# Kernel optimization log

Measured on AMD Instinct MI355X. Metric: run time of the kernel, lower is better.

## Reference

```python
import jax, jax.numpy as jnp
import numpy as np

B, L, K = 2, 4096, 32
DIM, PE_DIM, HEADS, DIM_HEAD = 256, 64, 8, 32
INNER = HEADS * DIM_HEAD
SIGMA_INIT = 3.0


def setup_inputs() -> dict:
    key = jax.random.key(0)
    ks = jax.random.split(key, 10)
    x = jax.random.normal(ks[0], (B, L, DIM), dtype=jnp.float32)
    topk_indices = jax.random.randint(ks[1], (B, L, K), 0, L)
    rpe = jax.random.normal(ks[2], (B, L, K, PE_DIM), dtype=jnp.float32)
    distances = jax.random.uniform(ks[3], (B, L, K), dtype=jnp.float32)
    s = lambda fan_in: 1.0 / np.sqrt(fan_in)
    Wq = jax.random.uniform(ks[4], (DIM, INNER), jnp.float32, -s(DIM), s(DIM))
    Wk = jax.random.uniform(ks[5], (DIM + PE_DIM, INNER), jnp.float32, -s(DIM + PE_DIM), s(DIM + PE_DIM))
    Wv = jax.random.uniform(ks[6], (DIM + PE_DIM, INNER), jnp.float32, -s(DIM + PE_DIM), s(DIM + PE_DIM))
    Wout = jax.random.uniform(ks[7], (INNER, DIM), jnp.float32, -s(INNER), s(INNER))
    b_out = jax.random.uniform(ks[8], (DIM,), jnp.float32, -s(INNER), s(INNER))
    log_sigma = jnp.full((HEADS,), np.log(SIGMA_INIT), dtype=jnp.float32)
    return {"x": x, "topk_indices": topk_indices, "rpe": rpe, "distances": distances,
            "Wq": Wq, "Wk": Wk, "Wv": Wv, "Wout": Wout, "b_out": b_out, "log_sigma": log_sigma}


def reference(x, topk_indices, rpe, distances, Wq, Wk, Wv, Wout, b_out, log_sigma):
    H, Dh = HEADS, DIM_HEAD
    scale = Dh ** -0.5
    # per-batch neighbor gather: [B, L, k, D]
    neighbors = jax.vmap(lambda xb, ib: xb[ib])(x, topk_indices)
    context = jnp.concatenate([neighbors, rpe], axis=-1)  # [B, L, k, D+pe]
    Bv, Lv = x.shape[0], x.shape[1]
    Q = (x @ Wq).reshape(Bv, Lv, H, Dh)                       # [B, L, H, d]
    Kt = (context @ Wk).reshape(Bv, Lv, -1, H, Dh)            # [B, L, k, H, d]
    Vt = (context @ Wv).reshape(Bv, Lv, -1, H, Dh)            # [B, L, k, H, d]
    attn = jnp.einsum('blhd,blkhd->bhlk', Q, Kt) * scale      # [B, H, L, k]
    sigma_sq = jnp.exp(log_sigma) ** 2                        # [H]
    bias = -(distances ** 2)[:, None] / (2.0 * sigma_sq[None, :, None, None])
    attn = jax.nn.softmax(attn + bias, axis=-1)
    out = jnp.einsum('bhlk,blkhd->blhd', attn, Vt).reshape(Bv, Lv, H * Dh)
    return out @ Wout + b_out
```

## Files before the change

### kernel.cpp

```cpp
#include <hip/hip_runtime.h>
#include <cstddef>

#define NROWS 8192
#define LLEN  4096
#define KNBR  32
#define DIMX  256
#define PEDIM 64
#define NH    8
#define DHD   32
#define QKVLD 768

__global__ __launch_bounds__(256)
void qkv_gemm(const float* __restrict__ x, const float* __restrict__ Wq,
              const float* __restrict__ Wk, const float* __restrict__ Wv,
              float* __restrict__ QKV)
{
    __shared__ float As[16][64];
    __shared__ float Bs[16][64];
    const int t  = threadIdx.x;
    const int m0 = blockIdx.x * 64;
    const int n0 = blockIdx.y * 64;
    const float* Bmat = (n0 < 256) ? Wq : (n0 < 512) ? Wk : Wv;
    const int nb = n0 & 255;
    const int tx = t & 15, ty = t >> 4;
    const int lm = t >> 2, lk4 = (t & 3) * 4;
    const int bn = t & 63, bk = t >> 6;

    float acc[4][4];
#pragma unroll
    for (int i = 0; i < 4; ++i)
#pragma unroll
        for (int j = 0; j < 4; ++j) acc[i][j] = 0.f;

    for (int k0 = 0; k0 < DIMX; k0 += 16) {
        float4 av = *(const float4*)&x[(size_t)(m0 + lm) * DIMX + k0 + lk4];
        As[lk4 + 0][lm] = av.x;
        As[lk4 + 1][lm] = av.y;
        As[lk4 + 2][lm] = av.z;
        As[lk4 + 3][lm] = av.w;
#pragma unroll
        for (int p = 0; p < 4; ++p)
            Bs[bk + p * 4][bn] = Bmat[(size_t)(k0 + bk + p * 4) * 256 + nb + bn];
        __syncthreads();
#pragma unroll
        for (int kk = 0; kk < 16; ++kk) {
            float4 a = *(const float4*)&As[kk][ty * 4];
            float4 b = *(const float4*)&Bs[kk][tx * 4];
            float ar[4] = {a.x, a.y, a.z, a.w};
            float br[4] = {b.x, b.y, b.z, b.w};
#pragma unroll
            for (int i = 0; i < 4; ++i)
#pragma unroll
                for (int j = 0; j < 4; ++j)
                    acc[i][j] += ar[i] * br[j];
        }
        __syncthreads();
    }
#pragma unroll
    for (int i = 0; i < 4; ++i)
        *(float4*)&QKV[(size_t)(m0 + ty * 4 + i) * QKVLD + n0 + tx * 4] =
            make_float4(acc[i][0], acc[i][1], acc[i][2], acc[i][3]);
}

__global__ __launch_bounds__(256)
void gemm_nn(const float* __restrict__ A, int lda,
             const float* __restrict__ B, int ldb,
             const float* __restrict__ bias,
             float* __restrict__ C, int ldc, int Kd)
{
    __shared__ float As[16][64];
    __shared__ float Bs[16][64];
    const int t  = threadIdx.x;
    const int m0 = blockIdx.x * 64;
    const int n0 = blockIdx.y * 64;
    const int tx = t & 15, ty = t >> 4;
    const int lm = t >> 2, lk4 = (t & 3) * 4;
    const int bn = t & 63, bk = t >> 6;

    float acc[4][4];
#pragma unroll
    for (int i = 0; i < 4; ++i)
#pragma unroll
        for (int j = 0; j < 4; ++j) acc[i][j] = 0.f;

    for (int k0 = 0; k0 < Kd; k0 += 16) {
        float4 av = *(const float4*)&A[(size_t)(m0 + lm) * lda + k0 + lk4];
        As[lk4 + 0][lm] = av.x;
        As[lk4 + 1][lm] = av.y;
        As[lk4 + 2][lm] = av.z;
        As[lk4 + 3][lm] = av.w;
#pragma unroll
        for (int p = 0; p < 4; ++p)
            Bs[bk + p * 4][bn] = B[(size_t)(k0 + bk + p * 4) * ldb + n0 + bn];
        __syncthreads();
#pragma unroll
        for (int kk = 0; kk < 16; ++kk) {
            float4 a = *(const float4*)&As[kk][ty * 4];
            float4 b = *(const float4*)&Bs[kk][tx * 4];
            float ar[4] = {a.x, a.y, a.z, a.w};
            float br[4] = {b.x, b.y, b.z, b.w};
#pragma unroll
            for (int i = 0; i < 4; ++i)
#pragma unroll
                for (int j = 0; j < 4; ++j)
                    acc[i][j] += ar[i] * br[j];
        }
        __syncthreads();
    }
#pragma unroll
    for (int i = 0; i < 4; ++i) {
        const int row = m0 + ty * 4 + i;
        float ov[4];
#pragma unroll
        for (int j = 0; j < 4; ++j)
            ov[j] = acc[i][j] + (bias ? bias[n0 + tx * 4 + j] : 0.f);
        *(float4*)&C[(size_t)row * ldc + n0 + tx * 4] =
            make_float4(ov[0], ov[1], ov[2], ov[3]);
    }
}

__global__ __launch_bounds__(256)
void attn_fused(const float* __restrict__ QKV, const int* __restrict__ topk,
                const float* __restrict__ rpe, const float* __restrict__ dist,
                const float* __restrict__ lsig,
                const float* __restrict__ Wk, const float* __restrict__ Wv,
                float* __restrict__ O)
{
    __shared__ float Qs[4][256];
    __shared__ float Tr[4][NH][PEDIM];
    __shared__ float As2[4][KNBR][NH];
    __shared__ float Us[4][NH][PEDIM];
    __shared__ float Ox[4][256];

    const int t    = threadIdx.x;
    const int w    = t >> 6;
    const int lane = t & 63;
    const int r0   = blockIdx.x * 4;
    const int r    = r0 + w;
    const int b    = r >> 12;
    const float scale = 0.17677669529663687f;

    *(float4*)&Qs[w][lane * 4] = *(const float4*)&QKV[(size_t)r * QKVLD + lane * 4];
    __syncthreads();

    {
        const int h = t >> 5, cl = t & 31;
#pragma unroll
        for (int cc = 0; cc < 2; ++cc) {
            const int c = cl + cc * 32;
            const float4* wp = (const float4*)&Wk[(size_t)(256 + c) * 256 + h * 32];
            float4 wk[8];
#pragma unroll
            for (int j = 0; j < 8; ++j) wk[j] = wp[j];
#pragma unroll
            for (int i = 0; i < 4; ++i) {
                const float4* qp = (const float4*)&Qs[i][h * 32];
                float s = 0.f;
#pragma unroll
                for (int j = 0; j < 8; ++j) {
                    float4 q = qp[j];
                    s += q.x * wk[j].x + q.y * wk[j].y + q.z * wk[j].z + q.w * wk[j].w;
                }
                Tr[i][h][c] = s;
            }
        }
    }
    __syncthreads();

    const int kk = lane & 31, hh = lane >> 5;
    const int myidx = topk[r * KNBR + kk];
    const float* ktrow = &QKV[(size_t)(b * LLEN + myidx) * QKVLD + 256];
    const float* rrow  = &rpe[((size_t)r * KNBR + kk) * PEDIM];

    float acc4[4] = {0.f, 0.f, 0.f, 0.f};
#pragma unroll
    for (int i = 0; i < 4; ++i) {
        const int h = hh * 4 + i;
        const float4* qp = (const float4*)&Qs[w][h * 32];
        const float4* kp = (const float4*)&ktrow[h * 32];
        float s = 0.f;
#pragma unroll
        for (int j = 0; j < 8; ++j) {
            float4 q = qp[j]; float4 kv = kp[j];
            s += q.x * kv.x + q.y * kv.y + q.z * kv.z + q.w * kv.w;
        }
        acc4[i] = s;
    }
    for (int c4 = 0; c4 < 16; ++c4) {
        float4 rv = ((const float4*)rrow)[c4];
#pragma unroll
        for (int i = 0; i < 4; ++i) {
            float4 tv = *(const float4*)&Tr[w][hh * 4 + i][c4 * 4];
            acc4[i] += rv.x * tv.x + rv.y * tv.y + rv.z * tv.z + rv.w * tv.w;
        }
    }
    {
        float dd = dist[r * KNBR + kk];
        const float d2 = dd * dd;
#pragma unroll
        for (int i = 0; i < 4; ++i) {
            const int h = hh * 4 + i;
            const float sig2 = __expf(2.f * lsig[h]);
            float lg = acc4[i] * scale - d2 / (2.f * sig2);
            float mx = lg;
#pragma unroll
            for (int m = 16; m >= 1; m >>= 1)
                mx = fmaxf(mx, __shfl_xor(mx, m, 64));
            float pv = __expf(lg - mx);
            float sm = pv;
#pragma unroll
            for (int m = 16; m >= 1; m >>= 1)
                sm += __shfl_xor(sm, m, 64);
            As2[w][kk][h] = pv / sm;
        }
    }

    {
        const int h2 = lane >> 3;
        const int* tkp = &topk[r * KNBR];
        float4 ox = make_float4(0.f, 0.f, 0.f, 0.f);
        for (int k = 0; k < KNBR; ++k) {
            const int ik = tkp[k];
            const float aw = As2[w][k][h2];
            float4 vv = *(const float4*)&QKV[(size_t)(b * LLEN + ik) * QKVLD + 512 + lane * 4];
            ox.x += aw * vv.x; ox.y += aw * vv.y;
            ox.z += aw * vv.z; ox.w += aw * vv.w;
        }
        *(float4*)&Ox[w][lane * 4] = ox;
    }

    {
        float u[NH] = {0.f, 0.f, 0.f, 0.f, 0.f, 0.f, 0.f, 0.f};
        for (int k = 0; k < KNBR; ++k) {
            const float rv = rpe[((size_t)r * KNBR + k) * PEDIM + lane];
            float4 a0 = *(const float4*)&As2[w][k][0];
            float4 a1 = *(const float4*)&As2[w][k][4];
            u[0] += a0.x * rv; u[1] += a0.y * rv; u[2] += a0.z * rv; u[3] += a0.w * rv;
            u[4] += a1.x * rv; u[5] += a1.y * rv; u[6] += a1.z * rv; u[7] += a1.w * rv;
        }
#pragma unroll
        for (int h = 0; h < NH; ++h) Us[w][h][lane] = u[h];
    }
    __syncthreads();

    {
        const int n = t, hn = n >> 5;
        float accp[4] = {0.f, 0.f, 0.f, 0.f};
        for (int c4 = 0; c4 < 16; ++c4) {
            const float wv0 = Wv[(size_t)(256 + c4 * 4 + 0) * 256 + n];
            const float wv1 = Wv[(size_t)(256 + c4 * 4 + 1) * 256 + n];
            const float wv2 = Wv[(size_t)(256 + c4 * 4 + 2) * 256 + n];
            const float wv3 = Wv[(size_t)(256 + c4 * 4 + 3) * 256 + n];
#pragma unroll
            for (int i = 0; i < 4; ++i) {
                float4 uv = *(const float4*)&Us[i][hn][c4 * 4];
                accp[i] += uv.x * wv0 + uv.y * wv1 + uv.z * wv2 + uv.w * wv3;
            }
        }
#pragma unroll
        for (int i = 0; i < 4; ++i)
            O[(size_t)(r0 + i) * QKVLD + n] = Ox[i][n] + accp[i];
    }
}

extern "C" void kernel_launch(void* const* d_in, const int* in_sizes, int n_in,
                              void* d_out, int out_size, void* d_ws, size_t ws_size,
                              hipStream_t stream)
{
    const float* x     = (const float*)d_in[0];
    const int*   topk  = (const int*)  d_in[1];
    const float* rpe   = (const float*)d_in[2];
    const float* dist  = (const float*)d_in[3];
    const float* Wq    = (const float*)d_in[4];
    const float* Wk    = (const float*)d_in[5];
    const float* Wv    = (const float*)d_in[6];
    const float* Wout  = (const float*)d_in[7];
    const float* b_out = (const float*)d_in[8];
    const float* lsig  = (const float*)d_in[9];
    float* out = (float*)d_out;

    float* QKV = (float*)d_ws;

    qkv_gemm<<<dim3(NROWS / 64, QKVLD / 64), 256, 0, stream>>>(x, Wq, Wk, Wv, QKV);
    attn_fused<<<NROWS / 4, 256, 0, stream>>>(QKV, topk, rpe, dist, lsig, Wk, Wv, QKV);
    gemm_nn<<<dim3(NROWS / 64, DIMX / 64), 256, 0, stream>>>(
        QKV, QKVLD, Wout, 256, b_out, out, 256, DIMX);
}
```

Before: 274.7 us.

## Unify GEMMs with larger register tiles and prefetch; shrink attention blocks, stage rpe/topk in LDS

Replaces the two 64x64 GEMM kernels with one 128x64-tile kernel that computes an 8x8 register block per thread, prefetches the next K slice into registers, and pads shared memory. The attention kernel drops to two rows per 128-thread block. It stages rpe rows and topk indices in shared memory so they are read from global memory once, and reuses shared buffers. The aim is more arithmetic per shared-memory load in the GEMMs and fewer redundant global loads in attention. The costs are higher register pressure in the GEMM and more attention blocks, each reloading the Wk and Wv slices with reuse across only two rows.

```diff
diff --git a/kernel.cpp b/kernel.cpp
--- a/kernel.cpp
+++ b/kernel.cpp
@@ -7,195 +7,175 @@
 #define DIMX  256
 #define PEDIM 64
 #define NH    8
-#define DHD   32
 #define QKVLD 768
 
-__global__ __launch_bounds__(256)
-void qkv_gemm(const float* __restrict__ x, const float* __restrict__ Wq,
-              const float* __restrict__ Wk, const float* __restrict__ Wv,
-              float* __restrict__ QKV)
+__global__ __launch_bounds__(128)
+void gemm_f32(const float* __restrict__ A, int lda,
+              const float* __restrict__ B0, const float* __restrict__ B1,
+              const float* __restrict__ B2, int ldb,
+              const float* __restrict__ bias,
+              float* __restrict__ C, int ldc, int Kd)
 {
-    __shared__ float As[16][64];
-    __shared__ float Bs[16][64];
+    __shared__ float As[16][132];
+    __shared__ float Bs[16][68];
     const int t  = threadIdx.x;
-    const int m0 = blockIdx.x * 64;
-    const int n0 = blockIdx.y * 64;
-    const float* Bmat = (n0 < 256) ? Wq : (n0 < 512) ? Wk : Wv;
-    const int nb = n0 & 255;
-    const int tx = t & 15, ty = t >> 4;
-    const int lm = t >> 2, lk4 = (t & 3) * 4;
-    const int bn = t & 63, bk = t >> 6;
-
-    float acc[4][4];
-#pragma unroll
-    for (int i = 0; i < 4; ++i)
-#pragma unroll
-        for (int j = 0; j < 4; ++j) acc[i][j] = 0.f;
-
-    for (int k0 = 0; k0 < DIMX; k0 += 16) {
-        float4 av = *(const float4*)&x[(size_t)(m0 + lm) * DIMX + k0 + lk4];
-        As[lk4 + 0][lm] = av.x;
-        As[lk4 + 1][lm] = av.y;
-        As[lk4 + 2][lm] = av.z;
-        As[lk4 + 3][lm] = av.w;
-#pragma unroll
-        for (int p = 0; p < 4; ++p)
-            Bs[bk + p * 4][bn] = Bmat[(size_t)(k0 + bk + p * 4) * 256 + nb + bn];
+    const int m0 = blockIdx.x * 128;
+    const int by = blockIdx.y;
+    const int n0 = by * 64;
+    const float* Bm = (by < 4) ? B0 : (by < 8) ? B1 : B2;
+    const int nb = (by & 3) * 64;
+    const int tx = t & 7, ty = t >> 3;
+
+    float acc[8][8] = {};
+    float4 av[4], bv[2];
+    const float* Arow = A + (size_t)(m0 + t) * lda;
+
+#pragma unroll
+    for (int q = 0; q < 4; ++q) av[q] = *(const float4*)&Arow[q * 4];
+#pragma unroll
+    for (int p = 0; p < 2; ++p) {
+        const int id = t + p * 128, kq = id >> 4, c4 = id & 15;
+        bv[p] = *(const float4*)&Bm[(size_t)kq * ldb + nb + c4 * 4];
+    }
+
+    for (int k0 = 0; k0 < Kd; k0 += 16) {
+#pragma unroll
+        for (int q = 0; q < 4; ++q) {
+            As[q * 4 + 0][t] = av[q].x; As[q * 4 + 1][t] = av[q].y;
+            As[q * 4 + 2][t] = av[q].z; As[q * 4 + 3][t] = av[q].w;
+        }
+#pragma unroll
+        for (int p = 0; p < 2; ++p) {
+            const int id = t + p * 128, kq = id >> 4, c4 = id & 15;
+            *(float4*)&Bs[kq][c4 * 4] = bv[p];
+        }
         __syncthreads();
+        if (k0 + 16 < Kd) {
+#pragma unroll
+            for (int q = 0; q < 4; ++q)
+                av[q] = *(const float4*)&Arow[k0 + 16 + q * 4];
+#pragma unroll
+            for (int p = 0; p < 2; ++p) {
+                const int id = t + p * 128, kq = id >> 4, c4 = id & 15;
+                bv[p] = *(const float4*)&Bm[(size_t)(k0 + 16 + kq) * ldb + nb + c4 * 4];
+            }
+        }
 #pragma unroll
         for (int kk = 0; kk < 16; ++kk) {
-            float4 a = *(const float4*)&As[kk][ty * 4];
-            float4 b = *(const float4*)&Bs[kk][tx * 4];
-            float ar[4] = {a.x, a.y, a.z, a.w};
-            float br[4] = {b.x, b.y, b.z, b.w};
-#pragma unroll
-            for (int i = 0; i < 4; ++i)
-#pragma unroll
-                for (int j = 0; j < 4; ++j)
+            float4 a0 = *(const float4*)&As[kk][ty * 4];
+            float4 a1 = *(const float4*)&As[kk][64 + ty * 4];
+            float4 b0 = *(const float4*)&Bs[kk][tx * 4];
+            float4 b1 = *(const float4*)&Bs[kk][32 + tx * 4];
+            float ar[8] = {a0.x, a0.y, a0.z, a0.w, a1.x, a1.y, a1.z, a1.w};
+            float br[8] = {b0.x, b0.y, b0.z, b0.w, b1.x, b1.y, b1.z, b1.w};
+#pragma unroll
+            for (int i = 0; i < 8; ++i)
+#pragma unroll
+                for (int j = 0; j < 8; ++j)
                     acc[i][j] += ar[i] * br[j];
         }
         __syncthreads();
     }
-#pragma unroll
-    for (int i = 0; i < 4; ++i)
-        *(float4*)&QKV[(size_t)(m0 + ty * 4 + i) * QKVLD + n0 + tx * 4] =
-            make_float4(acc[i][0], acc[i][1], acc[i][2], acc[i][3]);
+
+#pragma unroll
+    for (int ih = 0; ih < 2; ++ih)
+#pragma unroll
+    for (int i = 0; i < 4; ++i) {
+        const int row = m0 + ih * 64 + ty * 4 + i;
+#pragma unroll
+        for (int jh = 0; jh < 2; ++jh) {
+            const int col = n0 + jh * 32 + tx * 4;
+            float4 o;
+            o.x = acc[ih * 4 + i][jh * 4 + 0] + (bias ? bias[col + 0] : 0.f);
+            o.y = acc[ih * 4 + i][jh * 4 + 1] + (bias ? bias[col + 1] : 0.f);
+            o.z = acc[ih * 4 + i][jh * 4 + 2] + (bias ? bias[col + 2] : 0.f);
+            o.w = acc[ih * 4 + i][jh * 4 + 3] + (bias ? bias[col + 3] : 0.f);
+            *(float4*)&C[(size_t)row * ldc + col] = o;
+        }
+    }
 }
 
-__global__ __launch_bounds__(256)
-void gemm_nn(const float* __restrict__ A, int lda,
-             const float* __restrict__ B, int ldb,
-             const float* __restrict__ bias,
-             float* __restrict__ C, int ldc, int Kd)
-{
-    __shared__ float As[16][64];
-    __shared__ float Bs[16][64];
-    const int t  = threadIdx.x;
-    const int m0 = blockIdx.x * 64;
-    const int n0 = blockIdx.y * 64;
-    const int tx = t & 15, ty = t >> 4;
-    const int lm = t >> 2, lk4 = (t & 3) * 4;
-    const int bn = t & 63, bk = t >> 6;
-
-    float acc[4][4];
-#pragma unroll
-    for (int i = 0; i < 4; ++i)
-#pragma unroll
-        for (int j = 0; j < 4; ++j) acc[i][j] = 0.f;
-
-    for (int k0 = 0; k0 < Kd; k0 += 16) {
-        float4 av = *(const float4*)&A[(size_t)(m0 + lm) * lda + k0 + lk4];
-        As[lk4 + 0][lm] = av.x;
-        As[lk4 + 1][lm] = av.y;
-        As[lk4 + 2][lm] = av.z;
-        As[lk4 + 3][lm] = av.w;
-#pragma unroll
-        for (int p = 0; p < 4; ++p)
-            Bs[bk + p * 4][bn] = B[(size_t)(k0 + bk + p * 4) * ldb + n0 + bn];
-        __syncthreads();
-#pragma unroll
-        for (int kk = 0; kk < 16; ++kk) {
-            float4 a = *(const float4*)&As[kk][ty * 4];
-            float4 b = *(const float4*)&Bs[kk][tx * 4];
-            float ar[4] = {a.x, a.y, a.z, a.w};
-            float br[4] = {b.x, b.y, b.z, b.w};
-#pragma unroll
-            for (int i = 0; i < 4; ++i)
-#pragma unroll
-                for (int j = 0; j < 4; ++j)
-                    acc[i][j] += ar[i] * br[j];
-        }
-        __syncthreads();
-    }
-#pragma unroll
-    for (int i = 0; i < 4; ++i) {
-        const int row = m0 + ty * 4 + i;
-        float ov[4];
-#pragma unroll
-        for (int j = 0; j < 4; ++j)
-            ov[j] = acc[i][j] + (bias ? bias[n0 + tx * 4 + j] : 0.f);
-        *(float4*)&C[(size_t)row * ldc + n0 + tx * 4] =
-            make_float4(ov[0], ov[1], ov[2], ov[3]);
-    }
-}
-
-__global__ __launch_bounds__(256)
-void attn_fused(const float* __restrict__ QKV, const int* __restrict__ topk,
+__global__ __launch_bounds__(128)
+void attn_fused(const float* QKV, const int* __restrict__ topk,
                 const float* __restrict__ rpe, const float* __restrict__ dist,
                 const float* __restrict__ lsig,
                 const float* __restrict__ Wk, const float* __restrict__ Wv,
-                float* __restrict__ O)
+                float* O)
 {
-    __shared__ float Qs[4][256];
-    __shared__ float Tr[4][NH][PEDIM];
-    __shared__ float As2[4][KNBR][NH];
-    __shared__ float Us[4][NH][PEDIM];
-    __shared__ float Ox[4][256];
-
-    const int t    = threadIdx.x;
-    const int w    = t >> 6;
-    const int lane = t & 63;
-    const int r0   = blockIdx.x * 4;
-    const int r    = r0 + w;
-    const int b    = r >> 12;
+    __shared__ float QsOx[2][256];
+    __shared__ float TrUs[2][NH][68];
+    __shared__ float As2[2][KNBR][8];
+    __shared__ float rpeS[2][KNBR][68];
+    __shared__ int   tkS[2][KNBR];
+
+    const int t = threadIdx.x, w = t >> 6, lane = t & 63;
+    const int r0 = blockIdx.x * 2, r = r0 + w;
+    const int b = r >> 12;
     const float scale = 0.17677669529663687f;
 
-    *(float4*)&Qs[w][lane * 4] = *(const float4*)&QKV[(size_t)r * QKVLD + lane * 4];
+    *(float4*)&QsOx[w][lane * 4] = *(const float4*)&QKV[(size_t)r * QKVLD + lane * 4];
+#pragma unroll
+    for (int p = 0; p < 8; ++p) {
+        const int g = p * 64 + lane;
+        const int k = g >> 4, c4 = g & 15;
+        *(float4*)&rpeS[w][k][c4 * 4] =
+            *(const float4*)&rpe[((size_t)r * KNBR + k) * PEDIM + c4 * 4];
+    }
+    if (lane < KNBR) tkS[w][lane] = topk[r * KNBR + lane];
     __syncthreads();
 
     {
-        const int h = t >> 5, cl = t & 31;
-#pragma unroll
-        for (int cc = 0; cc < 2; ++cc) {
-            const int c = cl + cc * 32;
-            const float4* wp = (const float4*)&Wk[(size_t)(256 + c) * 256 + h * 32];
-            float4 wk[8];
-#pragma unroll
-            for (int j = 0; j < 8; ++j) wk[j] = wp[j];
+        const int h = t >> 4, cl = t & 15;
+#pragma unroll
+        for (int i = 0; i < 2; ++i) {
+            float4 q[8];
+#pragma unroll
+            for (int j = 0; j < 8; ++j)
+                q[j] = *(const float4*)&QsOx[i][h * 32 + j * 4];
+#pragma unroll
+            for (int cc = 0; cc < 4; ++cc) {
+                const int c = cl + cc * 16;
+                const float4* wp = (const float4*)&Wk[(size_t)(256 + c) * 256 + h * 32];
+                float s = 0.f;
+#pragma unroll
+                for (int j = 0; j < 8; ++j) {
+                    float4 wv_ = wp[j];
+                    s += q[j].x * wv_.x + q[j].y * wv_.y + q[j].z * wv_.z + q[j].w * wv_.w;
+                }
+                TrUs[i][h][c] = s;
+            }
+        }
+    }
+    __syncthreads();
+
+    const int kk = lane & 31, hh = lane >> 5;
+    {
+        const int myidx = tkS[w][kk];
+        const float* ktrow = &QKV[(size_t)(b * LLEN + myidx) * QKVLD + 256];
+        float acc4[4];
+#pragma unroll
+        for (int i = 0; i < 4; ++i) {
+            const int h = hh * 4 + i;
+            const float4* qp = (const float4*)&QsOx[w][h * 32];
+            const float4* kp = (const float4*)&ktrow[h * 32];
+            float s = 0.f;
+#pragma unroll
+            for (int j = 0; j < 8; ++j) {
+                float4 q = qp[j], kv = kp[j];
+                s += q.x * kv.x + q.y * kv.y + q.z * kv.z + q.w * kv.w;
+            }
+            acc4[i] = s;
+        }
+#pragma unroll 4
+        for (int c4 = 0; c4 < 16; ++c4) {
+            float4 rv = *(const float4*)&rpeS[w][kk][c4 * 4];
 #pragma unroll
             for (int i = 0; i < 4; ++i) {
-                const float4* qp = (const float4*)&Qs[i][h * 32];
-                float s = 0.f;
-#pragma unroll
-                for (int j = 0; j < 8; ++j) {
-                    float4 q = qp[j];
-                    s += q.x * wk[j].x + q.y * wk[j].y + q.z * wk[j].z + q.w * wk[j].w;
-                }
-                Tr[i][h][c] = s;
-            }
-        }
-    }
-    __syncthreads();
-
-    const int kk = lane & 31, hh = lane >> 5;
-    const int myidx = topk[r * KNBR + kk];
-    const float* ktrow = &QKV[(size_t)(b * LLEN + myidx) * QKVLD + 256];
-    const float* rrow  = &rpe[((size_t)r * KNBR + kk) * PEDIM];
-
-    float acc4[4] = {0.f, 0.f, 0.f, 0.f};
-#pragma unroll
-    for (int i = 0; i < 4; ++i) {
-        const int h = hh * 4 + i;
-        const float4* qp = (const float4*)&Qs[w][h * 32];
-        const float4* kp = (const float4*)&ktrow[h * 32];
-        float s = 0.f;
-#pragma unroll
-        for (int j = 0; j < 8; ++j) {
-            float4 q = qp[j]; float4 kv = kp[j];
-            s += q.x * kv.x + q.y * kv.y + q.z * kv.z + q.w * kv.w;
-        }
-        acc4[i] = s;
-    }
-    for (int c4 = 0; c4 < 16; ++c4) {
-        float4 rv = ((const float4*)rrow)[c4];
-#pragma unroll
-        for (int i = 0; i < 4; ++i) {
-            float4 tv = *(const float4*)&Tr[w][hh * 4 + i][c4 * 4];
-            acc4[i] += rv.x * tv.x + rv.y * tv.y + rv.z * tv.z + rv.w * tv.w;
-        }
-    }
-    {
-        float dd = dist[r * KNBR + kk];
+                float4 tv = *(const float4*)&TrUs[w][hh * 4 + i][c4 * 4];
+                acc4[i] += rv.x * tv.x + rv.y * tv.y + rv.z * tv.z + rv.w * tv.w;
+            }
+        }
+        const float dd = dist[r * KNBR + kk];
         const float d2 = dd * dd;
 #pragma unroll
         for (int i = 0; i < 4; ++i) {
@@ -217,49 +197,50 @@
 
     {
         const int h2 = lane >> 3;
-        const int* tkp = &topk[r * KNBR];
-        float4 ox = make_float4(0.f, 0.f, 0.f, 0.f);
+        const float* vbase = &QKV[(size_t)b * LLEN * QKVLD + 512 + lane * 4];
+        float4 ox = {0.f, 0.f, 0.f, 0.f};
+#pragma unroll 8
         for (int k = 0; k < KNBR; ++k) {
-            const int ik = tkp[k];
+            const int ik = tkS[w][k];
+            float4 vv = *(const float4*)&vbase[(size_t)ik * QKVLD];
             const float aw = As2[w][k][h2];
-            float4 vv = *(const float4*)&QKV[(size_t)(b * LLEN + ik) * QKVLD + 512 + lane * 4];
             ox.x += aw * vv.x; ox.y += aw * vv.y;
             ox.z += aw * vv.z; ox.w += aw * vv.w;
         }
-        *(float4*)&Ox[w][lane * 4] = ox;
-    }
-
-    {
-        float u[NH] = {0.f, 0.f, 0.f, 0.f, 0.f, 0.f, 0.f, 0.f};
+        *(float4*)&QsOx[w][lane * 4] = ox;
+    }
+
+    {
+        float u[8] = {};
+#pragma unroll 8
         for (int k = 0; k < KNBR; ++k) {
-            const float rv = rpe[((size_t)r * KNBR + k) * PEDIM + lane];
+            const float rv = rpeS[w][k][lane];
             float4 a0 = *(const float4*)&As2[w][k][0];
             float4 a1 = *(const float4*)&As2[w][k][4];
             u[0] += a0.x * rv; u[1] += a0.y * rv; u[2] += a0.z * rv; u[3] += a0.w * rv;
             u[4] += a1.x * rv; u[5] += a1.y * rv; u[6] += a1.z * rv; u[7] += a1.w * rv;
         }
 #pragma unroll
-        for (int h = 0; h < NH; ++h) Us[w][h][lane] = u[h];
+        for (int h = 0; h < NH; ++h) TrUs[w][h][lane] = u[h];
     }
     __syncthreads();
 
-    {
-        const int n = t, hn = n >> 5;
-        float accp[4] = {0.f, 0.f, 0.f, 0.f};
+#pragma unroll
+    for (int half = 0; half < 2; ++half) {
+        const int n = t + half * 128;
+        const int hn = n >> 5;
+        float accp0 = 0.f, accp1 = 0.f;
+#pragma unroll 4
         for (int c4 = 0; c4 < 16; ++c4) {
-            const float wv0 = Wv[(size_t)(256 + c4 * 4 + 0) * 256 + n];
-            const float wv1 = Wv[(size_t)(256 + c4 * 4 + 1) * 256 + n];
-            const float wv2 = Wv[(size_t)(256 + c4 * 4 + 2) * 256 + n];
-            const float wv3 = Wv[(size_t)(256 + c4 * 4 + 3) * 256 + n];
-#pragma unroll
-            for (int i = 0; i < 4; ++i) {
-                float4 uv = *(const float4*)&Us[i][hn][c4 * 4];
-                accp[i] += uv.x * wv0 + uv.y * wv1 + uv.z * wv2 + uv.w * wv3;
-            }
-        }
-#pragma unroll
-        for (int i = 0; i < 4; ++i)
-            O[(size_t)(r0 + i) * QKVLD + n] = Ox[i][n] + accp[i];
+            float4 u0 = *(const float4*)&TrUs[0][hn][c4 * 4];
+            float4 u1 = *(const float4*)&TrUs[1][hn][c4 * 4];
+            const float* wvp = &Wv[(size_t)(256 + c4 * 4) * 256 + n];
+            const float w0 = wvp[0], w1 = wvp[256], w2 = wvp[512], w3 = wvp[768];
+            accp0 += u0.x * w0 + u0.y * w1 + u0.z * w2 + u0.w * w3;
+            accp1 += u1.x * w0 + u1.y * w1 + u1.z * w2 + u1.w * w3;
+        }
+        O[(size_t)(r0 + 0) * QKVLD + n] = QsOx[0][n] + accp0;
+        O[(size_t)(r0 + 1) * QKVLD + n] = QsOx[1][n] + accp1;
     }
 }
 
@@ -281,8 +262,9 @@
 
     float* QKV = (float*)d_ws;
 
-    qkv_gemm<<<dim3(NROWS / 64, QKVLD / 64), 256, 0, stream>>>(x, Wq, Wk, Wv, QKV);
-    attn_fused<<<NROWS / 4, 256, 0, stream>>>(QKV, topk, rpe, dist, lsig, Wk, Wv, QKV);
-    gemm_nn<<<dim3(NROWS / 64, DIMX / 64), 256, 0, stream>>>(
-        QKV, QKVLD, Wout, 256, b_out, out, 256, DIMX);
+    gemm_f32<<<dim3(NROWS / 128, QKVLD / 64), 128, 0, stream>>>(
+        x, DIMX, Wq, Wk, Wv, DIMX, nullptr, QKV, QKVLD, DIMX);
+    attn_fused<<<NROWS / 2, 128, 0, stream>>>(QKV, topk, rpe, dist, lsig, Wk, Wv, QKV);
+    gemm_f32<<<dim3(NROWS / 128, DIMX / 64), 128, 0, stream>>>(
+        QKV, QKVLD, Wout, Wout, Wout, DIMX, b_out, out, DIMX, DIMX);
 }
```

Result: slower. 419.4 us (+52.7%).
